# Performance work log

Hardware: AMD Instinct MI355X
Metric: run time of the kernel (lower is better)

## Reference

```python
import jax, jax.numpy as jnp
import numpy as np

DIM = 1024
HEADS = 16
HEAD_DIM = DIM // HEADS
NUM_FILTERS = 4
NUM_TAPS = 101
RES = 512

def setup_inputs() -> dict:
    key = jax.random.key(0)
    ks = jax.random.split(key, 5)
    B, S = 2, 2048
    x = jax.random.normal(ks[0], (B, S, DIM), dtype=jnp.float32)
    Wqkv = jax.random.normal(ks[1], (3 * DIM, DIM), dtype=jnp.float32) * (DIM ** -0.5)
    Wout = jax.random.normal(ks[2], (DIM, DIM), dtype=jnp.float32) * (DIM ** -0.5)
    Wpos = jax.random.normal(ks[3], (HEADS, NUM_FILTERS), dtype=jnp.float32) * 0.5
    coeffs = jax.random.normal(ks[4], (NUM_FILTERS, NUM_TAPS), dtype=jnp.float32) * 0.05
    return {"x": x, "Wqkv": Wqkv, "Wout": Wout, "Wpos": Wpos, "coeffs": coeffs}

def _fir_fft(c, sig):
    # c: (T,), sig: (R,) -> causal FFT convolution, first R samples
    R = sig.shape[0]
    L = R + c.shape[0] - 1
    out = jnp.fft.ifft(jnp.fft.fft(sig, n=L) * jnp.fft.fft(c, n=L)).real
    return out[:R]

def reference(x, Wqkv, Wout, Wpos, coeffs):
    B, S, D = x.shape
    scale = HEAD_DIM ** -0.5

    # filtered prototype table: (R, F)
    proto = jnp.linspace(0.0, 1.0, RES).astype(x.dtype)
    table = jax.vmap(_fir_fft, in_axes=(0, None))(coeffs, proto).T  # (R, F)

    # relative-distance index matrix (S, S), constants derived from static shape
    r = jnp.arange(S)
    rel = jnp.abs(r[None, :] - r[:, None]).astype(jnp.float32) / max(S - 1, 1)
    idx = jnp.clip(jnp.round(rel * (RES - 1)).astype(jnp.int32), 0, RES - 1)

    pos_feat = table[idx]                                   # (S, S, F)
    pos_bias = jnp.einsum('ijf,hf->hij', pos_feat, Wpos)    # (H, S, S)

    qkv = jnp.einsum('bsd,ed->bse', x, Wqkv)                # (B, S, 3D)
    q, k, v = jnp.split(qkv, 3, axis=-1)
    q = q.reshape(B, S, HEADS, HEAD_DIM)
    k = k.reshape(B, S, HEADS, HEAD_DIM)
    v = v.reshape(B, S, HEADS, HEAD_DIM)

    logits = jnp.einsum('bihd,bjhd->bhij', q, k) * scale + pos_bias[None]
    attn = jax.nn.softmax(logits, axis=-1)
    out = jnp.einsum('bhij,bjhd->bihd', attn, v).reshape(B, S, D)
    return jnp.einsum('bsd,ed->bse', out, Wout)
```

## Files before the change

### kernel.cpp

```cpp
#include <hip/hip_runtime.h>
#include <cstddef>

#define SEQ     2048
#define BATCH   2
#define DIMSZ   1024
#define HEADS   16
#define HDIM    64
#define E3      3072
#define RESN    512
#define NTAPS   101
#define NFILT   4
#define MROWS   (BATCH * SEQ)

typedef __attribute__((ext_vector_type(8))) short bf16x8;
typedef __attribute__((ext_vector_type(4))) float f32x4;

__device__ __forceinline__ unsigned short f2bf(float f) {
  unsigned u = __float_as_uint(f);
  u += 0x7fffu + ((u >> 16) & 1u);
  return (unsigned short)(u >> 16);
}
__device__ __forceinline__ float bf2f(unsigned short h) {
  return __uint_as_float(((unsigned)h) << 16);
}
__device__ __forceinline__ void split2(float f, unsigned short& h, unsigned short& l) {
  h = f2bf(f);
  l = f2bf(f - bf2f(h));
}

__global__ __launch_bounds__(256) void cvt_bf16_kern(
    const float* __restrict__ src, unsigned short* __restrict__ dst, int n)
{
  const int i = (blockIdx.x * 256 + threadIdx.x) * 8;
  if (i >= n) return;
  const float4 a = *(const float4*)(src + i);
  const float4 b = *(const float4*)(src + i + 4);
  ushort4 p = {f2bf(a.x), f2bf(a.y), f2bf(a.z), f2bf(a.w)};
  ushort4 q = {f2bf(b.x), f2bf(b.y), f2bf(b.z), f2bf(b.w)};
  *(ushort4*)(dst + i)     = p;
  *(ushort4*)(dst + i + 4) = q;
}

__global__ __launch_bounds__(256) void split_pair_kern(
    const float* __restrict__ src, unsigned short* __restrict__ hi,
    unsigned short* __restrict__ lo, int n)
{
  const int i = (blockIdx.x * 256 + threadIdx.x) * 4;
  if (i >= n) return;
  const float4 a = *(const float4*)(src + i);
  ushort4 h, l;
  split2(a.x, h.x, l.x); split2(a.y, h.y, l.y);
  split2(a.z, h.z, l.z); split2(a.w, h.w, l.w);
  *(ushort4*)(hi + i) = h;
  *(ushort4*)(lo + i) = l;
}

__global__ __launch_bounds__(256) void pbias_kernel(
    const float* __restrict__ coeffs, const float* __restrict__ Wpos,
    float* __restrict__ pbias)
{
  __shared__ float table[RESN][NFILT];
  __shared__ float wp[HEADS * NFILT];
  const int tid = threadIdx.x;
  if (tid < HEADS * NFILT) wp[tid] = Wpos[tid];
  for (int rf = tid; rf < RESN * NFILT; rf += 256) {
    const int r = rf >> 2, f = rf & 3;
    const int tmax = r < (NTAPS - 1) ? r : (NTAPS - 1);
    float s = 0.f;
    for (int t = 0; t <= tmax; ++t)
      s += coeffs[f * NTAPS + t] * ((float)(r - t) * (1.0f / (float)(RESN - 1)));
    table[r][f] = s;
  }
  __syncthreads();
  for (int hd = tid; hd < HEADS * SEQ; hd += 256) {
    const int h = hd >> 11, d = hd & (SEQ - 1);
    const float rel = (float)d / (float)(SEQ - 1);
    int idx = (int)rintf(rel * (float)(RESN - 1));
    idx = idx < 0 ? 0 : (idx > RESN - 1 ? RESN - 1 : idx);
    float s = 0.f;
#pragma unroll
    for (int f = 0; f < NFILT; ++f) s += table[idx][f] * wp[h * NFILT + f];
    pbias[hd] = s;
  }
}

__global__ __launch_bounds__(256) void gemm_bf16(
    const unsigned short* __restrict__ A, const unsigned short* __restrict__ B,
    unsigned short* __restrict__ C, int M, int N, int K)
{
  __shared__ unsigned short As[128][72];
  __shared__ unsigned short Bs[128][72];
  const int tid = threadIdx.x;
  const int lane = tid & 63;
  const int w = tid >> 6, wm = w >> 1, wn = w & 1;
  const int c = lane & 15, G = lane >> 4;
  const int m0 = blockIdx.y * 128, n0 = blockIdx.x * 128;

  f32x4 acc[4][4];
#pragma unroll
  for (int mf = 0; mf < 4; ++mf)
#pragma unroll
    for (int nf = 0; nf < 4; ++nf) acc[mf][nf] = (f32x4){0.f, 0.f, 0.f, 0.f};

  for (int k0 = 0; k0 < K; k0 += 64) {
    bf16x8 va[4], vb[4];
#pragma unroll
    for (int rep = 0; rep < 4; ++rep) {
      const int u = tid + rep * 256;
      const int row = u >> 3, s = u & 7;
      va[rep] = *(const bf16x8*)(A + (size_t)(m0 + row) * K + k0 + 8 * s);
      vb[rep] = *(const bf16x8*)(B + (size_t)(n0 + row) * K + k0 + 8 * s);
    }
    __syncthreads();
#pragma unroll
    for (int rep = 0; rep < 4; ++rep) {
      const int u = tid + rep * 256;
      const int row = u >> 3, s = u & 7;
      *(bf16x8*)&As[row][8 * s] = va[rep];
      *(bf16x8*)&Bs[row][8 * s] = vb[rep];
    }
    __syncthreads();
#pragma unroll
    for (int ks = 0; ks < 2; ++ks) {
      bf16x8 fa[4], fb[4];
#pragma unroll
      for (int mf = 0; mf < 4; ++mf)
        fa[mf] = *(const bf16x8*)&As[wm * 64 + 16 * mf + c][32 * ks + 8 * G];
#pragma unroll
      for (int nf = 0; nf < 4; ++nf)
        fb[nf] = *(const bf16x8*)&Bs[wn * 64 + 16 * nf + c][32 * ks + 8 * G];
#pragma unroll
      for (int nf = 0; nf < 4; ++nf)
#pragma unroll
        for (int mf = 0; mf < 4; ++mf)
          acc[mf][nf] = __builtin_amdgcn_mfma_f32_16x16x32_bf16(fa[mf], fb[nf], acc[mf][nf], 0, 0, 0);
    }
  }

#pragma unroll
  for (int mf = 0; mf < 4; ++mf)
#pragma unroll
    for (int nf = 0; nf < 4; ++nf)
#pragma unroll
      for (int r = 0; r < 4; ++r)
        C[(size_t)(m0 + wm * 64 + 16 * mf + 4 * G + r) * N + n0 + wn * 64 + 16 * nf + c] =
            f2bf(acc[mf][nf][r]);
}

__global__ __launch_bounds__(256) void gemm_split3(
    const unsigned short* __restrict__ Ah, const unsigned short* __restrict__ Al,
    const unsigned short* __restrict__ Bh, const unsigned short* __restrict__ Bl,
    float* __restrict__ C, int M, int N, int K)
{
  __shared__ unsigned short AhS[128][40], AlS[128][40];
  __shared__ unsigned short BhS[128][40], BlS[128][40];
  const int tid = threadIdx.x;
  const int lane = tid & 63;
  const int w = tid >> 6, wm = w >> 1, wn = w & 1;
  const int c = lane & 15, G = lane >> 4;
  const int m0 = blockIdx.y * 128, n0 = blockIdx.x * 128;

  f32x4 acc[4][4];
#pragma unroll
  for (int mf = 0; mf < 4; ++mf)
#pragma unroll
    for (int nf = 0; nf < 4; ++nf) acc[mf][nf] = (f32x4){0.f, 0.f, 0.f, 0.f};

  for (int k0 = 0; k0 < K; k0 += 32) {
    bf16x8 vah[2], val[2], vbh[2], vbl[2];
#pragma unroll
    for (int rep = 0; rep < 2; ++rep) {
      const int u = tid + rep * 256;
      const int row = u >> 2, s = u & 3;
      const size_t oa = (size_t)(m0 + row) * K + k0 + 8 * s;
      const size_t ob = (size_t)(n0 + row) * K + k0 + 8 * s;
      vah[rep] = *(const bf16x8*)(Ah + oa);
      val[rep] = *(const bf16x8*)(Al + oa);
      vbh[rep] = *(const bf16x8*)(Bh + ob);
      vbl[rep] = *(const bf16x8*)(Bl + ob);
    }
    __syncthreads();
#pragma unroll
    for (int rep = 0; rep < 2; ++rep) {
      const int u = tid + rep * 256;
      const int row = u >> 2, s = u & 3;
      *(bf16x8*)&AhS[row][8 * s] = vah[rep];
      *(bf16x8*)&AlS[row][8 * s] = val[rep];
      *(bf16x8*)&BhS[row][8 * s] = vbh[rep];
      *(bf16x8*)&BlS[row][8 * s] = vbl[rep];
    }
    __syncthreads();
    bf16x8 fah[4], fal[4];
#pragma unroll
    for (int mf = 0; mf < 4; ++mf) {
      fah[mf] = *(const bf16x8*)&AhS[wm * 64 + 16 * mf + c][8 * G];
      fal[mf] = *(const bf16x8*)&AlS[wm * 64 + 16 * mf + c][8 * G];
    }
#pragma unroll
    for (int nf = 0; nf < 4; ++nf) {
      const bf16x8 fbh = *(const bf16x8*)&BhS[wn * 64 + 16 * nf + c][8 * G];
      const bf16x8 fbl = *(const bf16x8*)&BlS[wn * 64 + 16 * nf + c][8 * G];
#pragma unroll
      for (int mf = 0; mf < 4; ++mf) {
        acc[mf][nf] = __builtin_amdgcn_mfma_f32_16x16x32_bf16(fah[mf], fbh, acc[mf][nf], 0, 0, 0);
        acc[mf][nf] = __builtin_amdgcn_mfma_f32_16x16x32_bf16(fah[mf], fbl, acc[mf][nf], 0, 0, 0);
        acc[mf][nf] = __builtin_amdgcn_mfma_f32_16x16x32_bf16(fal[mf], fbh, acc[mf][nf], 0, 0, 0);
      }
    }
  }

#pragma unroll
  for (int mf = 0; mf < 4; ++mf)
#pragma unroll
    for (int nf = 0; nf < 4; ++nf)
#pragma unroll
      for (int r = 0; r < 4; ++r)
        C[(size_t)(m0 + wm * 64 + 16 * mf + 4 * G + r) * N + n0 + wn * 64 + 16 * nf + c] =
            acc[mf][nf][r];
}

__global__ __launch_bounds__(256) void attn_pure(
    const unsigned short* __restrict__ qkv,
    const float* __restrict__ pbias,
    unsigned short* __restrict__ ao_hi,
    unsigned short* __restrict__ ao_lo)
{
  __shared__ unsigned short Kh[64][72];
  __shared__ unsigned short Vh[64][64];
  __shared__ unsigned short Ps[64][72];
  __shared__ float pb[SEQ];

  const int tid = threadIdx.x;
  const int lane = tid & 63;
  const int w = tid >> 6;
  const int c = lane & 15, G = lane >> 4;
  const int bh = blockIdx.y, b = bh >> 4, h = bh & 15;
  const int i0 = blockIdx.x * 64;
  const int i_glob = i0 + w * 16 + c;
  const float scale = 0.125f;

  for (int idx = tid * 4; idx < SEQ; idx += 1024)
    *(float4*)&pb[idx] = *(const float4*)(pbias + h * SEQ + idx);

  bf16x8 qb[2];
#pragma unroll
  for (int ks = 0; ks < 2; ++ks)
    qb[ks] = *(const bf16x8*)(qkv + (size_t)(b * SEQ + i_glob) * E3 + h * HDIM + 32 * ks + 8 * G);

  f32x4 oacc[4];
#pragma unroll
  for (int nf = 0; nf < 4; ++nf) oacc[nf] = (f32x4){0.f, 0.f, 0.f, 0.f};
  float mi = -1e30f, li = 0.f;

  const int vd8 = 8 * (tid & 7);
  const int vjp = 2 * (tid >> 3);

  for (int jt = 0; jt < SEQ / 64; ++jt) {
    const int j0 = jt * 64;
    const size_t rowK = (size_t)(b * SEQ + j0) * E3 + DIMSZ + h * HDIM;
    const size_t rowV = (size_t)(b * SEQ + j0) * E3 + 2 * DIMSZ + h * HDIM;

    bf16x8 kv[2];
#pragma unroll
    for (int rep = 0; rep < 2; ++rep) {
      const int u = tid + rep * 256;
      const int j = u >> 3, s = u & 7;
      kv[rep] = *(const bf16x8*)(qkv + rowK + (size_t)j * E3 + 8 * s);
    }
    const bf16x8 v0 = *(const bf16x8*)(qkv + rowV + (size_t)vjp * E3 + vd8);
    const bf16x8 v1 = *(const bf16x8*)(qkv + rowV + (size_t)(vjp + 1) * E3 + vd8);

    __syncthreads();

#pragma unroll
    for (int rep = 0; rep < 2; ++rep) {
      const int u = tid + rep * 256;
      const int j = u >> 3, s = u & 7;
      *(bf16x8*)&Kh[j][8 * s] = kv[rep];
    }
#pragma unroll
    for (int e = 0; e < 8; ++e) {
      const int d = vd8 + e;
      const unsigned pk = (unsigned)(unsigned short)v0[e] |
                          ((unsigned)(unsigned short)v1[e] << 16);
      const int colp = ((((vjp >> 3) ^ ((d >> 2) & 7)) << 3) | (vjp & 7));
      *(unsigned*)&Vh[d][colp] = pk;
    }
    __syncthreads();

    f32x4 st[4];
#pragma unroll
    for (int mf = 0; mf < 4; ++mf) st[mf] = (f32x4){0.f, 0.f, 0.f, 0.f};
#pragma unroll
    for (int ks = 0; ks < 2; ++ks)
#pragma unroll
      for (int mf = 0; mf < 4; ++mf) {
        const bf16x8 ka = *(const bf16x8*)&Kh[16 * mf + c][32 * ks + 8 * G];
        st[mf] = __builtin_amdgcn_mfma_f32_16x16x32_bf16(ka, qb[ks], st[mf], 0, 0, 0);
      }

    float p[16];
    float rm = -1e30f;
#pragma unroll
    for (int mf = 0; mf < 4; ++mf)
#pragma unroll
      for (int r = 0; r < 4; ++r) {
        const int j = j0 + 16 * mf + 4 * G + r;
        const int d = i_glob > j ? i_glob - j : j - i_glob;
        const float lg = fmaf(st[mf][r], scale, pb[d]);
        p[mf * 4 + r] = lg;
        rm = fmaxf(rm, lg);
      }
    rm = fmaxf(rm, __shfl_xor(rm, 16));
    rm = fmaxf(rm, __shfl_xor(rm, 32));
    const float newm = fmaxf(mi, rm);
    const float fr = __expf(mi - newm);
    float rs = 0.f;
#pragma unroll
    for (int t = 0; t < 16; ++t) {
      p[t] = __expf(p[t] - newm);
      rs += p[t];
    }
    rs += __shfl_xor(rs, 16);
    rs += __shfl_xor(rs, 32);
    li = li * fr + rs;
    mi = newm;
    float frr[4];
#pragma unroll
    for (int r = 0; r < 4; ++r) frr[r] = __shfl(fr, 20 * G + r);
#pragma unroll
    for (int nf = 0; nf < 4; ++nf)
#pragma unroll
      for (int r = 0; r < 4; ++r) oacc[nf][r] *= frr[r];

#pragma unroll
    for (int mf = 0; mf < 4; ++mf) {
      ushort4 ph = {f2bf(p[mf * 4 + 0]), f2bf(p[mf * 4 + 1]),
                    f2bf(p[mf * 4 + 2]), f2bf(p[mf * 4 + 3])};
      *(ushort4*)&Ps[16 * w + c][16 * mf + 4 * G] = ph;
    }

#pragma unroll
    for (int ks = 0; ks < 2; ++ks) {
      const bf16x8 pa = *(const bf16x8*)&Ps[16 * w + c][32 * ks + 8 * G];
#pragma unroll
      for (int nf = 0; nf < 4; ++nf) {
        const int d = 16 * nf + c;
        const int sl = ((4 * ks + G) ^ ((d >> 2) & 7)) << 3;
        const bf16x8 vb = *(const bf16x8*)&Vh[d][sl];
        oacc[nf] = __builtin_amdgcn_mfma_f32_16x16x32_bf16(pa, vb, oacc[nf], 0, 0, 0);
      }
    }
  }

  float rinv[4];
#pragma unroll
  for (int r = 0; r < 4; ++r) rinv[r] = 1.0f / __shfl(li, 20 * G + r);
#pragma unroll
  for (int nf = 0; nf < 4; ++nf)
#pragma unroll
    for (int r = 0; r < 4; ++r) {
      const float v = oacc[nf][r] * rinv[r];
      const size_t off = (size_t)(b * SEQ + i0 + 16 * w + 4 * G + r) * DIMSZ +
                         h * HDIM + 16 * nf + c;
      unsigned short vh, vl;
      split2(v, vh, vl);
      ao_hi[off] = vh;
      ao_lo[off] = vl;
    }
}

extern "C" void kernel_launch(void* const* d_in, const int* in_sizes, int n_in,
                              void* d_out, int out_size, void* d_ws, size_t ws_size,
                              hipStream_t stream) {
  const float* x      = (const float*)d_in[0];
  const float* Wqkv   = (const float*)d_in[1];
  const float* Wout   = (const float*)d_in[2];
  const float* Wpos   = (const float*)d_in[3];
  const float* coeffs = (const float*)d_in[4];
  float* out = (float*)d_out;

  unsigned short* qkv_bf  = (unsigned short*)d_ws;
  unsigned short* x_bf    = qkv_bf + (size_t)MROWS * E3;
  unsigned short* wqkv_bf = x_bf + (size_t)MROWS * DIMSZ;
  unsigned short* wout_h  = wqkv_bf + (size_t)E3 * DIMSZ;
  unsigned short* wout_l  = wout_h + (size_t)DIMSZ * DIMSZ;
  unsigned short* ao_h    = wout_l + (size_t)DIMSZ * DIMSZ;
  unsigned short* ao_l    = ao_h + (size_t)MROWS * DIMSZ;
  float* pbias = (float*)(ao_l + (size_t)MROWS * DIMSZ);

  const int nx = MROWS * DIMSZ;
  const int nw = E3 * DIMSZ;
  const int no = DIMSZ * DIMSZ;

  cvt_bf16_kern<<<nx / 2048, 256, 0, stream>>>(x, x_bf, nx);
  cvt_bf16_kern<<<nw / 2048, 256, 0, stream>>>(Wqkv, wqkv_bf, nw);
  split_pair_kern<<<no / 1024, 256, 0, stream>>>(Wout, wout_h, wout_l, no);
  pbias_kernel<<<1, 256, 0, stream>>>(coeffs, Wpos, pbias);

  dim3 g1(E3 / 128, MROWS / 128);
  gemm_bf16<<<g1, 256, 0, stream>>>(x_bf, wqkv_bf, qkv_bf, MROWS, E3, DIMSZ);

  dim3 g2(SEQ / 64, BATCH * HEADS);
  attn_pure<<<g2, 256, 0, stream>>>(qkv_bf, pbias, ao_h, ao_l);

  dim3 g3(DIMSZ / 128, MROWS / 128);
  gemm_split3<<<g3, 256, 0, stream>>>(ao_h, ao_l, wout_h, wout_l, out, MROWS, DIMSZ, DIMSZ);
}
```

Measured before the change: 332.9 us.

## Use direct global-to-LDS loads, XOR swizzles, exp2 softmax, parallel pbias

Both GEMMs and the attention K tile now stage through LDS with global_load_lds async copies instead of register round trips. The padded shared arrays are replaced with unpadded tiles, and XOR swizzles in the attention kernel avoid bank conflicts. Softmax uses exp2 with log2e folded into the scale and the bias, P is packed into bf16 pairs with a hardware conversion, and the bias kernel runs one block per head. The QKV GEMM drops to a K-step of 32, which doubles the barriers, and the unpadded GEMM tiles may cause LDS bank conflicts.

```diff
diff --git a/kernel.cpp b/kernel.cpp
--- a/kernel.cpp
+++ b/kernel.cpp
@@ -1,4 +1,5 @@
 #include <hip/hip_runtime.h>
+#include <hip/hip_bf16.h>
 #include <cstddef>
 
 #define SEQ     2048
@@ -11,6 +12,7 @@
 #define NTAPS   101
 #define NFILT   4
 #define MROWS   (BATCH * SEQ)
+#define LOG2E   1.44269504088896340736f
 
 typedef __attribute__((ext_vector_type(8))) short bf16x8;
 typedef __attribute__((ext_vector_type(4))) float f32x4;
@@ -26,6 +28,16 @@
 __device__ __forceinline__ void split2(float f, unsigned short& h, unsigned short& l) {
   h = f2bf(f);
   l = f2bf(f - bf2f(h));
+}
+__device__ __forceinline__ unsigned pkbf(float a, float b) {
+  __hip_bfloat162 t = __float22bfloat162_rn(float2{a, b});
+  union { __hip_bfloat162 h; unsigned u; } cv; cv.h = t;
+  return cv.u;
+}
+__device__ __forceinline__ void async16(void* lds, const void* g) {
+  __builtin_amdgcn_global_load_lds(
+      (const __attribute__((address_space(1))) unsigned int*)g,
+      (__attribute__((address_space(3))) unsigned int*)lds, 16, 0, 0);
 }
 
 __global__ __launch_bounds__(256) void cvt_bf16_kern(
@@ -57,12 +69,11 @@
 
 __global__ __launch_bounds__(256) void pbias_kernel(
     const float* __restrict__ coeffs, const float* __restrict__ Wpos,
-    float* __restrict__ pbias)
+    float* __restrict__ pbias2)
 {
   __shared__ float table[RESN][NFILT];
-  __shared__ float wp[HEADS * NFILT];
+  const int h = blockIdx.x;
   const int tid = threadIdx.x;
-  if (tid < HEADS * NFILT) wp[tid] = Wpos[tid];
   for (int rf = tid; rf < RESN * NFILT; rf += 256) {
     const int r = rf >> 2, f = rf & 3;
     const int tmax = r < (NTAPS - 1) ? r : (NTAPS - 1);
@@ -72,15 +83,17 @@
     table[r][f] = s;
   }
   __syncthreads();
-  for (int hd = tid; hd < HEADS * SEQ; hd += 256) {
-    const int h = hd >> 11, d = hd & (SEQ - 1);
+  float wp[NFILT];
+#pragma unroll
+  for (int f = 0; f < NFILT; ++f) wp[f] = Wpos[h * NFILT + f];
+  for (int d = tid; d < SEQ; d += 256) {
     const float rel = (float)d / (float)(SEQ - 1);
     int idx = (int)rintf(rel * (float)(RESN - 1));
     idx = idx < 0 ? 0 : (idx > RESN - 1 ? RESN - 1 : idx);
     float s = 0.f;
 #pragma unroll
-    for (int f = 0; f < NFILT; ++f) s += table[idx][f] * wp[h * NFILT + f];
-    pbias[hd] = s;
+    for (int f = 0; f < NFILT; ++f) s += table[idx][f] * wp[f];
+    pbias2[h * SEQ + d] = s * LOG2E;
   }
 }
 
@@ -88,53 +101,46 @@
     const unsigned short* __restrict__ A, const unsigned short* __restrict__ B,
     unsigned short* __restrict__ C, int M, int N, int K)
 {
-  __shared__ unsigned short As[128][72];
-  __shared__ unsigned short Bs[128][72];
+  __shared__ unsigned short As[128][32];
+  __shared__ unsigned short Bs[128][32];
   const int tid = threadIdx.x;
   const int lane = tid & 63;
   const int w = tid >> 6, wm = w >> 1, wn = w & 1;
   const int c = lane & 15, G = lane >> 4;
   const int m0 = blockIdx.y * 128, n0 = blockIdx.x * 128;
 
+  const int srow = lane >> 2;
+  const int scol = (lane & 3) << 3;
+
   f32x4 acc[4][4];
 #pragma unroll
   for (int mf = 0; mf < 4; ++mf)
 #pragma unroll
     for (int nf = 0; nf < 4; ++nf) acc[mf][nf] = (f32x4){0.f, 0.f, 0.f, 0.f};
 
-  for (int k0 = 0; k0 < K; k0 += 64) {
-    bf16x8 va[4], vb[4];
-#pragma unroll
-    for (int rep = 0; rep < 4; ++rep) {
-      const int u = tid + rep * 256;
-      const int row = u >> 3, s = u & 7;
-      va[rep] = *(const bf16x8*)(A + (size_t)(m0 + row) * K + k0 + 8 * s);
-      vb[rep] = *(const bf16x8*)(B + (size_t)(n0 + row) * K + k0 + 8 * s);
-    }
-    __syncthreads();
-#pragma unroll
-    for (int rep = 0; rep < 4; ++rep) {
-      const int u = tid + rep * 256;
-      const int row = u >> 3, s = u & 7;
-      *(bf16x8*)&As[row][8 * s] = va[rep];
-      *(bf16x8*)&Bs[row][8 * s] = vb[rep];
-    }
-    __syncthreads();
-#pragma unroll
-    for (int ks = 0; ks < 2; ++ks) {
-      bf16x8 fa[4], fb[4];
+  for (int k0 = 0; k0 < K; k0 += 32) {
+    __syncthreads();
+#pragma unroll
+    for (int r = 0; r < 2; ++r) {
+      const int chunk = r * 4 + w;
+      const int row = (chunk << 4) + srow;
+      async16(&As[chunk << 4][0], A + (size_t)(m0 + row) * K + k0 + scol);
+      async16(&Bs[chunk << 4][0], B + (size_t)(n0 + row) * K + k0 + scol);
+    }
+    __syncthreads();
+
+    bf16x8 fa[4], fb[4];
+#pragma unroll
+    for (int mf = 0; mf < 4; ++mf)
+      fa[mf] = *(const bf16x8*)&As[wm * 64 + 16 * mf + c][8 * G];
+#pragma unroll
+    for (int nf = 0; nf < 4; ++nf)
+      fb[nf] = *(const bf16x8*)&Bs[wn * 64 + 16 * nf + c][8 * G];
+#pragma unroll
+    for (int nf = 0; nf < 4; ++nf)
 #pragma unroll
       for (int mf = 0; mf < 4; ++mf)
-        fa[mf] = *(const bf16x8*)&As[wm * 64 + 16 * mf + c][32 * ks + 8 * G];
-#pragma unroll
-      for (int nf = 0; nf < 4; ++nf)
-        fb[nf] = *(const bf16x8*)&Bs[wn * 64 + 16 * nf + c][32 * ks + 8 * G];
-#pragma unroll
-      for (int nf = 0; nf < 4; ++nf)
-#pragma unroll
-        for (int mf = 0; mf < 4; ++mf)
-          acc[mf][nf] = __builtin_amdgcn_mfma_f32_16x16x32_bf16(fa[mf], fb[nf], acc[mf][nf], 0, 0, 0);
-    }
+        acc[mf][nf] = __builtin_amdgcn_mfma_f32_16x16x32_bf16(fa[mf], fb[nf], acc[mf][nf], 0, 0, 0);
   }
 
 #pragma unroll
@@ -152,14 +158,17 @@
     const unsigned short* __restrict__ Bh, const unsigned short* __restrict__ Bl,
     float* __restrict__ C, int M, int N, int K)
 {
-  __shared__ unsigned short AhS[128][40], AlS[128][40];
-  __shared__ unsigned short BhS[128][40], BlS[128][40];
+  __shared__ unsigned short AhS[128][32], AlS[128][32];
+  __shared__ unsigned short BhS[128][32], BlS[128][32];
   const int tid = threadIdx.x;
   const int lane = tid & 63;
   const int w = tid >> 6, wm = w >> 1, wn = w & 1;
   const int c = lane & 15, G = lane >> 4;
   const int m0 = blockIdx.y * 128, n0 = blockIdx.x * 128;
 
+  const int srow = lane >> 2;
+  const int scol = (lane & 3) << 3;
+
   f32x4 acc[4][4];
 #pragma unroll
   for (int mf = 0; mf < 4; ++mf)
@@ -167,29 +176,20 @@
     for (int nf = 0; nf < 4; ++nf) acc[mf][nf] = (f32x4){0.f, 0.f, 0.f, 0.f};
 
   for (int k0 = 0; k0 < K; k0 += 32) {
-    bf16x8 vah[2], val[2], vbh[2], vbl[2];
-#pragma unroll
-    for (int rep = 0; rep < 2; ++rep) {
-      const int u = tid + rep * 256;
-      const int row = u >> 2, s = u & 3;
-      const size_t oa = (size_t)(m0 + row) * K + k0 + 8 * s;
-      const size_t ob = (size_t)(n0 + row) * K + k0 + 8 * s;
-      vah[rep] = *(const bf16x8*)(Ah + oa);
-      val[rep] = *(const bf16x8*)(Al + oa);
-      vbh[rep] = *(const bf16x8*)(Bh + ob);
-      vbl[rep] = *(const bf16x8*)(Bl + ob);
-    }
-    __syncthreads();
-#pragma unroll
-    for (int rep = 0; rep < 2; ++rep) {
-      const int u = tid + rep * 256;
-      const int row = u >> 2, s = u & 3;
-      *(bf16x8*)&AhS[row][8 * s] = vah[rep];
-      *(bf16x8*)&AlS[row][8 * s] = val[rep];
-      *(bf16x8*)&BhS[row][8 * s] = vbh[rep];
-      *(bf16x8*)&BlS[row][8 * s] = vbl[rep];
-    }
-    __syncthreads();
+    __syncthreads();
+#pragma unroll
+    for (int r = 0; r < 2; ++r) {
+      const int chunk = r * 4 + w;
+      const int row = (chunk << 4) + srow;
+      const size_t oa = (size_t)(m0 + row) * K + k0 + scol;
+      const size_t ob = (size_t)(n0 + row) * K + k0 + scol;
+      async16(&AhS[chunk << 4][0], Ah + oa);
+      async16(&AlS[chunk << 4][0], Al + oa);
+      async16(&BhS[chunk << 4][0], Bh + ob);
+      async16(&BlS[chunk << 4][0], Bl + ob);
+    }
+    __syncthreads();
+
     bf16x8 fah[4], fal[4];
 #pragma unroll
     for (int mf = 0; mf < 4; ++mf) {
@@ -221,13 +221,13 @@
 
 __global__ __launch_bounds__(256) void attn_pure(
     const unsigned short* __restrict__ qkv,
-    const float* __restrict__ pbias,
+    const float* __restrict__ pbias2,
     unsigned short* __restrict__ ao_hi,
     unsigned short* __restrict__ ao_lo)
 {
-  __shared__ unsigned short Kh[64][72];
+  __shared__ unsigned short Kh[64][64];
   __shared__ unsigned short Vh[64][64];
-  __shared__ unsigned short Ps[64][72];
+  __shared__ unsigned short Ps[64][64];
   __shared__ float pb[SEQ];
 
   const int tid = threadIdx.x;
@@ -237,10 +237,10 @@
   const int bh = blockIdx.y, b = bh >> 4, h = bh & 15;
   const int i0 = blockIdx.x * 64;
   const int i_glob = i0 + w * 16 + c;
-  const float scale = 0.125f;
+  const float scale2 = 0.125f * LOG2E;
 
   for (int idx = tid * 4; idx < SEQ; idx += 1024)
-    *(float4*)&pb[idx] = *(const float4*)(pbias + h * SEQ + idx);
+    *(float4*)&pb[idx] = *(const float4*)(pbias2 + h * SEQ + idx);
 
   bf16x8 qb[2];
 #pragma unroll
@@ -254,37 +254,34 @@
 
   const int vd8 = 8 * (tid & 7);
   const int vjp = 2 * (tid >> 3);
+
+  const int klrow = lane >> 3;
+  const int klsl  = lane & 7;
 
   for (int jt = 0; jt < SEQ / 64; ++jt) {
     const int j0 = jt * 64;
     const size_t rowK = (size_t)(b * SEQ + j0) * E3 + DIMSZ + h * HDIM;
     const size_t rowV = (size_t)(b * SEQ + j0) * E3 + 2 * DIMSZ + h * HDIM;
 
-    bf16x8 kv[2];
-#pragma unroll
-    for (int rep = 0; rep < 2; ++rep) {
-      const int u = tid + rep * 256;
-      const int j = u >> 3, s = u & 7;
-      kv[rep] = *(const bf16x8*)(qkv + rowK + (size_t)j * E3 + 8 * s);
-    }
     const bf16x8 v0 = *(const bf16x8*)(qkv + rowV + (size_t)vjp * E3 + vd8);
     const bf16x8 v1 = *(const bf16x8*)(qkv + rowV + (size_t)(vjp + 1) * E3 + vd8);
 
     __syncthreads();
 
 #pragma unroll
-    for (int rep = 0; rep < 2; ++rep) {
-      const int u = tid + rep * 256;
-      const int j = u >> 3, s = u & 7;
-      *(bf16x8*)&Kh[j][8 * s] = kv[rep];
+    for (int r = 0; r < 2; ++r) {
+      const int chunk = r * 4 + w;
+      const int krow = (chunk << 3) + klrow;
+      const int ksl = klsl ^ (krow & 7);
+      async16(&Kh[chunk << 3][0], qkv + rowK + (size_t)krow * E3 + 8 * ksl);
     }
 #pragma unroll
     for (int e = 0; e < 8; ++e) {
       const int d = vd8 + e;
       const unsigned pk = (unsigned)(unsigned short)v0[e] |
                           ((unsigned)(unsigned short)v1[e] << 16);
-      const int colp = ((((vjp >> 3) ^ ((d >> 2) & 7)) << 3) | (vjp & 7));
-      *(unsigned*)&Vh[d][colp] = pk;
+      const int col = (((vjp >> 3) ^ (d & 7)) << 3) | (vjp & 7);
+      *(unsigned*)&Vh[d][col] = pk;
     }
     __syncthreads();
 
@@ -295,7 +292,8 @@
     for (int ks = 0; ks < 2; ++ks)
 #pragma unroll
       for (int mf = 0; mf < 4; ++mf) {
-        const bf16x8 ka = *(const bf16x8*)&Kh[16 * mf + c][32 * ks + 8 * G];
+        const int sr = (4 * ks + G) ^ (c & 7);
+        const bf16x8 ka = *(const bf16x8*)&Kh[16 * mf + c][8 * sr];
         st[mf] = __builtin_amdgcn_mfma_f32_16x16x32_bf16(ka, qb[ks], st[mf], 0, 0, 0);
       }
 
@@ -307,18 +305,18 @@
       for (int r = 0; r < 4; ++r) {
         const int j = j0 + 16 * mf + 4 * G + r;
         const int d = i_glob > j ? i_glob - j : j - i_glob;
-        const float lg = fmaf(st[mf][r], scale, pb[d]);
+        const float lg = fmaf(st[mf][r], scale2, pb[d]);
         p[mf * 4 + r] = lg;
         rm = fmaxf(rm, lg);
       }
     rm = fmaxf(rm, __shfl_xor(rm, 16));
     rm = fmaxf(rm, __shfl_xor(rm, 32));
     const float newm = fmaxf(mi, rm);
-    const float fr = __expf(mi - newm);
+    const float fr = exp2f(mi - newm);
     float rs = 0.f;
 #pragma unroll
     for (int t = 0; t < 16; ++t) {
-      p[t] = __expf(p[t] - newm);
+      p[t] = exp2f(p[t] - newm);
       rs += p[t];
     }
     rs += __shfl_xor(rs, 16);
@@ -335,19 +333,21 @@
 
 #pragma unroll
     for (int mf = 0; mf < 4; ++mf) {
-      ushort4 ph = {f2bf(p[mf * 4 + 0]), f2bf(p[mf * 4 + 1]),
-                    f2bf(p[mf * 4 + 2]), f2bf(p[mf * 4 + 3])};
-      *(ushort4*)&Ps[16 * w + c][16 * mf + 4 * G] = ph;
+      const int sw = (2 * mf + (G >> 1)) ^ (c & 7);
+      uint2 pw = {pkbf(p[4 * mf + 0], p[4 * mf + 1]),
+                  pkbf(p[4 * mf + 2], p[4 * mf + 3])};
+      *(uint2*)&Ps[16 * w + c][8 * sw + 4 * (G & 1)] = pw;
     }
 
 #pragma unroll
     for (int ks = 0; ks < 2; ++ks) {
-      const bf16x8 pa = *(const bf16x8*)&Ps[16 * w + c][32 * ks + 8 * G];
+      const int spr = (4 * ks + G) ^ (c & 7);
+      const bf16x8 pa = *(const bf16x8*)&Ps[16 * w + c][8 * spr];
 #pragma unroll
       for (int nf = 0; nf < 4; ++nf) {
         const int d = 16 * nf + c;
-        const int sl = ((4 * ks + G) ^ ((d >> 2) & 7)) << 3;
-        const bf16x8 vb = *(const bf16x8*)&Vh[d][sl];
+        const int sv = (4 * ks + G) ^ (d & 7);
+        const bf16x8 vb = *(const bf16x8*)&Vh[d][8 * sv];
         oacc[nf] = __builtin_amdgcn_mfma_f32_16x16x32_bf16(pa, vb, oacc[nf], 0, 0, 0);
       }
     }
@@ -387,7 +387,7 @@
   unsigned short* wout_l  = wout_h + (size_t)DIMSZ * DIMSZ;
   unsigned short* ao_h    = wout_l + (size_t)DIMSZ * DIMSZ;
   unsigned short* ao_l    = ao_h + (size_t)MROWS * DIMSZ;
-  float* pbias = (float*)(ao_l + (size_t)MROWS * DIMSZ);
+  float* pbias2 = (float*)(ao_l + (size_t)MROWS * DIMSZ);
 
   const int nx = MROWS * DIMSZ;
   const int nw = E3 * DIMSZ;
@@ -396,13 +396,13 @@
   cvt_bf16_kern<<<nx / 2048, 256, 0, stream>>>(x, x_bf, nx);
   cvt_bf16_kern<<<nw / 2048, 256, 0, stream>>>(Wqkv, wqkv_bf, nw);
   split_pair_kern<<<no / 1024, 256, 0, stream>>>(Wout, wout_h, wout_l, no);
-  pbias_kernel<<<1, 256, 0, stream>>>(coeffs, Wpos, pbias);
+  pbias_kernel<<<HEADS, 256, 0, stream>>>(coeffs, Wpos, pbias2);
 
   dim3 g1(E3 / 128, MROWS / 128);
   gemm_bf16<<<g1, 256, 0, stream>>>(x_bf, wqkv_bf, qkv_bf, MROWS, E3, DIMSZ);
 
   dim3 g2(SEQ / 64, BATCH * HEADS);
-  attn_pure<<<g2, 256, 0, stream>>>(qkv_bf, pbias, ao_h, ao_l);
+  attn_pure<<<g2, 256, 0, stream>>>(qkv_bf, pbias2, ao_h, ao_l);
 
   dim3 g3(DIMSZ / 128, MROWS / 128);
   gemm_split3<<<g3, 256, 0, stream>>>(ao_h, ao_l, wout_h, wout_l, out, MROWS, DIMSZ, DIMSZ);
```

Result: no change. 337.4 us (+1.3%).
